# Performance work log

Hardware: AMD Instinct MI355X
Metric: run time of the kernel (lower is better)

## Reference

```python
import jax, jax.numpy as jnp
import numpy as np

H = 512    # hidden size
NF = 512   # num_factor
B, S = 128, 64
D0, D1 = 1536, 2048


def setup_inputs() -> dict:
    key = jax.random.key(0)
    ks = jax.random.split(key, 14)
    stdv = 1.0 / np.sqrt(H)
    u = lambda k, shape: jax.random.uniform(k, shape, jnp.float32, -stdv, stdv)
    return {
        "x0": jax.random.normal(ks[0], (B, S, D0), jnp.float32),  # auxiliary stream (skip_info=1)
        "x1": jax.random.normal(ks[1], (B, S, D1), jnp.float32),  # main encoded stream
        # SVD_Weights for stream 0 (num_gate=2, no individual part) -> weight_fh
        "wa0": u(ks[2], (2 * H, NF)),
        "wb0": jax.random.uniform(ks[3], (NF, 1), jnp.float32, 1 - stdv, 1 + stdv),
        "wc0": u(ks[4], (NF, D0)),
        "b0": u(ks[5], (2 * H,)),
        # SVD_Weights for stream 1 (num_gate=2 shared + individual) -> weight_ih
        "wa1": u(ks[6], (2 * H, NF)),
        "wb1": jax.random.uniform(ks[7], (NF, 1), jnp.float32, 1 - stdv, 1 + stdv),
        "wc1": u(ks[8], (NF, D1)),
        "b1": u(ks[9], (2 * H,)),
        "iw1": u(ks[10], (H, D1)),
        "ib1": u(ks[11], (H,)),
        # GRU hidden-to-hidden params
        "whh": u(ks[12], (3 * H, H)),
        "bhh": u(ks[13], (3 * H,)),
    }


def _svd_weight(wa, wb, wc):
    # tag = [[1.]] (length_tag == 1)  ->  mid = wb @ tag = wb[:, 0]
    # W = wa @ diag(mid) @ wc
    return (wa * wb[:, 0][None, :]) @ wc


def reference(x0, x1, wa0, wb0, wc0, b0, wa1, wb1, wc1, b1, iw1, ib1, whh, bhh):
    bsz = x1.shape[0]
    # get_all_params for stream 1: [2H shared gates; H individual n-gate]
    w_ih = jnp.concatenate([_svd_weight(wa1, wb1, wc1), iw1], axis=0)  # [3H, D1]
    b_ih = jnp.concatenate([b1, ib1], axis=0)                          # [3H]
    # get_shared_params for stream 0: auxiliary gate contributions
    w_fh = _svd_weight(wa0, wb0, wc0)                                  # [2H, D0]

    # Precompute all input-side projections (time-parallel GEMMs)
    gi = jnp.einsum('bsd,gd->bsg', x1, w_ih) + b_ih   # [B,S,3H]
    gf = jnp.einsum('bsd,gd->bsg', x0, w_fh) + b0     # [B,S,2H]
    i_r, i_i, i_n = jnp.split(gi, 3, axis=-1)
    f_r, f_i = jnp.split(gf, 2, axis=-1)

    def step(hx, xs):
        ir, ii, inn, fr, fi = xs
        gh = hx @ whh.T + bhh
        h_r, h_i, h_n = jnp.split(gh, 3, axis=-1)
        r = jax.nn.sigmoid(ir + h_r + fr)
        z = jax.nn.sigmoid(ii + h_i + fi)
        n = jnp.tanh(inn + r * h_n)
        hy = n + z * (hx - n)
        return hy, hy

    xs = tuple(jnp.swapaxes(a, 0, 1) for a in (i_r, i_i, i_n, f_r, f_i))  # time-major
    h0 = jnp.zeros((bsz, H), x1.dtype)
    hT, out = jax.lax.scan(step, h0, xs)
    return jnp.swapaxes(out, 0, 1), hT  # ([B,S,H], [B,H])
```

## Files before the change

### kernel.cpp

```cpp
#include <hip/hip_runtime.h>

#define AS1 __attribute__((address_space(1)))
#define AS3 __attribute__((address_space(3)))

typedef __attribute__((ext_vector_type(8))) short short8;
typedef __attribute__((ext_vector_type(4))) float f32x4;
typedef __attribute__((ext_vector_type(4))) int int4v;
typedef unsigned long long u64;

static __device__ __forceinline__ unsigned short f2bf(float f) {
    unsigned u = __builtin_bit_cast(unsigned, f);
    u += 0x7FFFu + ((u >> 16) & 1u);
    return (unsigned short)(u >> 16);
}


__global__ void cvt_bf16_kernel(const float* __restrict__ in,
                                unsigned short* __restrict__ out, int n8) {
    int i = blockIdx.x * blockDim.x + threadIdx.x;
    int stride = gridDim.x * blockDim.x;
    for (; i < n8; i += stride) {
        const float4* p = (const float4*)in + 2 * (size_t)i;
        float4 a = p[0], b = p[1];
        short8 o;
        o[0] = f2bf(a.x); o[1] = f2bf(a.y); o[2] = f2bf(a.z); o[3] = f2bf(a.w);
        o[4] = f2bf(b.x); o[5] = f2bf(b.y); o[6] = f2bf(b.z); o[7] = f2bf(b.w);
        *(short8*)(out + 8 * (size_t)i) = o;
    }
}

__global__ void wab_kernel(const float* __restrict__ wa, const float* __restrict__ wb,
                           unsigned short* __restrict__ out, int n8) {
    int i = blockIdx.x * blockDim.x + threadIdx.x;
    int stride = gridDim.x * blockDim.x;
    for (; i < n8; i += stride) {
        int base = i * 8;
        int k = base & 511;
        const float4* pa = (const float4*)(wa + base);
        const float4* pb = (const float4*)(wb + k);
        float4 a0 = pa[0], a1 = pa[1], b0 = pb[0], b1 = pb[1];
        short8 o;
        o[0] = f2bf(a0.x * b0.x); o[1] = f2bf(a0.y * b0.y);
        o[2] = f2bf(a0.z * b0.z); o[3] = f2bf(a0.w * b0.w);
        o[4] = f2bf(a1.x * b1.x); o[5] = f2bf(a1.y * b1.y);
        o[6] = f2bf(a1.z * b1.z); o[7] = f2bf(a1.w * b1.w);
        *(short8*)(out + 8 * (size_t)i) = o;
    }
}

__global__ void wcT_kernel(const float* __restrict__ wc,
                           unsigned short* __restrict__ out, int N) {
    int i = blockIdx.x * blockDim.x + threadIdx.x;
    int total = N * 512;
    int stride = gridDim.x * blockDim.x;
    for (; i < total; i += stride) {
        int n = i >> 9, k = i & 511;
        out[i] = f2bf(wc[(size_t)k * N + n]);
    }
}

__global__ void bih_kernel(const float* __restrict__ b1, const float* __restrict__ ib1,
                           float* __restrict__ out) {
    int i = blockIdx.x * blockDim.x + threadIdx.x;
    if (i < 1536) out[i] = (i < 1024) ? b1[i] : ib1[i - 1024];
}

__global__ void scan_init_kernel(unsigned short* __restrict__ hbf,
                                 unsigned* __restrict__ ctrl) {
    int i = blockIdx.x * blockDim.x + threadIdx.x;
    if (i < 65536) hbf[i] = 0;
    if (i < 256) ctrl[i] = 0;
}


template <typename OutT, bool BIAS>
__global__ __launch_bounds__(256) void gemm_nt_kernel(
    const unsigned short* __restrict__ A, const unsigned short* __restrict__ B,
    OutT* __restrict__ C, const float* __restrict__ bias, int K, int ldC) {
    __shared__ __align__(16) unsigned short As[128 * 64];
    __shared__ __align__(16) unsigned short Bs[128 * 64];
    const int tid = threadIdx.x;
    const int wave = tid >> 6, lane = tid & 63;
    const long bm = (long)blockIdx.x * 128, bn = (long)blockIdx.y * 128;
    const int wr = (wave >> 1) * 64, wc = (wave & 1) * 64;
    f32x4 acc[4][4] = {};

    const int srow = tid >> 3;
    const int scol = (tid & 7) * 8;
    const unsigned short* Ag = A + bm * K + scol;
    const unsigned short* Bg = B + bn * K + scol;

    for (int kt = 0; kt < K; kt += 64) {
        __syncthreads();
#pragma unroll
        for (int i = 0; i < 4; ++i) {
            __builtin_amdgcn_global_load_lds(
                (const AS1 void*)(Ag + (long)(i * 32 + srow) * K + kt),
                (AS3 void*)(As + i * 2048 + wave * 512), 16, 0, 0);
        }
#pragma unroll
        for (int i = 0; i < 4; ++i) {
            __builtin_amdgcn_global_load_lds(
                (const AS1 void*)(Bg + (long)(i * 32 + srow) * K + kt),
                (AS3 void*)(Bs + i * 2048 + wave * 512), 16, 0, 0);
        }
        __syncthreads();
#pragma unroll
        for (int kk = 0; kk < 2; ++kk) {
            const int ko = kk * 32 + (lane >> 4) * 8;
            short8 af[4], bfr[4];
#pragma unroll
            for (int mi = 0; mi < 4; ++mi)
                af[mi] = *(const short8*)(As + (wr + mi * 16 + (lane & 15)) * 64 + ko);
#pragma unroll
            for (int ni = 0; ni < 4; ++ni)
                bfr[ni] = *(const short8*)(Bs + (wc + ni * 16 + (lane & 15)) * 64 + ko);
#pragma unroll
            for (int mi = 0; mi < 4; ++mi)
#pragma unroll
                for (int ni = 0; ni < 4; ++ni)
                    acc[mi][ni] = __builtin_amdgcn_mfma_f32_16x16x32_bf16(
                        af[mi], bfr[ni], acc[mi][ni], 0, 0, 0);
        }
    }

    const int rbase = (lane >> 4) * 4;
    const int cbase = lane & 15;
#pragma unroll
    for (int mi = 0; mi < 4; ++mi) {
#pragma unroll
        for (int ni = 0; ni < 4; ++ni) {
            long gc = bn + wc + ni * 16 + cbase;
            float bv = BIAS ? bias[gc] : 0.f;
#pragma unroll
            for (int j = 0; j < 4; ++j) {
                long gr = bm + wr + mi * 16 + rbase + j;
                float v = acc[mi][ni][j] + bv;
                if constexpr (sizeof(OutT) == 2)
                    C[gr * ldC + gc] = (OutT)f2bf(v);
                else
                    C[gr * ldC + gc] = v;
            }
        }
    }
}


__global__ __launch_bounds__(256, 1) void gru_scan_kernel(
    unsigned short* __restrict__ hbuf,
    const unsigned short* __restrict__ whh,
    const float* __restrict__ bhh,
    const float* __restrict__ gi, const float* __restrict__ gf,
    float* __restrict__ out, float* __restrict__ hT,
    unsigned* __restrict__ ctrl) {
    __shared__ __align__(16) unsigned short h_lds[16 * 512];
    __shared__ __align__(16) float gis[48 * 68];
    __shared__ __align__(16) float gfs[32 * 68];
    __shared__ unsigned fast_sh;

    const int tid = threadIdx.x;
    const int lane = tid & 63;
    const int wv = tid >> 6;
    const int bid = blockIdx.x;
    const int team = bid & 7;
    const int member = bid >> 3;
    const int r0 = team * 16;
    const int cb = member * 64;
    const int c0 = cb + wv * 16;
    const int lrow = lane & 15;
    const int q = lane >> 4;

    unsigned* flags = ctrl;
    unsigned* xcds = ctrl + 64;
    unsigned* probes = ctrl + 128;

    short8 wf[3][16];
#pragma unroll
    for (int g = 0; g < 3; ++g)
#pragma unroll
        for (int kk = 0; kk < 16; ++kk)
            wf[g][kk] = *(const short8*)(whh + (size_t)(g * 512 + c0 + lrow) * 512 + kk * 32 + q * 8);

    unsigned my_xcc;
    asm volatile("s_getreg_b32 %0, hwreg(20, 0, 32)" : "=s"(my_xcc));
    if (tid == 0) {
        probes[bid] = 0x5A5A0000u + (unsigned)bid;
        asm volatile("s_waitcnt vmcnt(0)" ::: "memory");
        __hip_atomic_store(&xcds[bid], my_xcc + 1u,
                           __ATOMIC_RELAXED, __HIP_MEMORY_SCOPE_AGENT);
    }
    {
        unsigned ok = 1;
        if (tid < 8) {
            int tb = tid * 8 + team;
            unsigned xv;
            do {
                xv = __hip_atomic_load(&xcds[tb], __ATOMIC_RELAXED,
                                       __HIP_MEMORY_SCOPE_AGENT);
                if (xv == 0) __builtin_amdgcn_s_sleep(1);
            } while (xv == 0);
            unsigned pv = *(volatile const unsigned*)&probes[tb];
            ok = (xv == my_xcc + 1u) && (pv == 0x5A5A0000u + (unsigned)tb);
        }
        ok = __all((int)ok) ? 1u : 0u;
        if (tid == 0) fast_sh = ok;
        __syncthreads();
    }
    const bool fast = fast_sh != 0;

    const int hc = c0 + lrow;
    const float br = bhh[hc], bz = bhh[512 + hc], bn_ = bhh[1024 + hc];
    const int rb = r0 + q * 4;
    const int lc = wv * 16 + lrow;
    float hprev[4] = {0.f, 0.f, 0.f, 0.f};

    const int chunk_sub = tid >> 4;
    const int u4 = (tid & 15) * 4;
    float4 sl[5];
    auto slab_load = [&](int t) {
#pragma unroll
        for (int k = 0; k < 5; ++k) {
            int chunk = k * 16 + chunk_sub;
            const float* p;
            if (chunk < 48) {
                int bbq = chunk / 3, g = chunk - bbq * 3;
                p = gi + ((size_t)(r0 + bbq) * 64 + t) * 1536 + g * 512 + cb + u4;
            } else {
                int c2 = chunk - 48, bbq = c2 >> 1, g2 = c2 & 1;
                p = gf + ((size_t)(r0 + bbq) * 64 + t) * 1024 + g2 * 512 + cb + u4;
            }
            sl[k] = *(const float4*)p;
        }
    };
    slab_load(0);

    const int srow = tid >> 4;
    const int cpos = tid & 15;
    const int sw = (srow & 7) << 4;

    for (int t = 0; t < 64; ++t) {
        const unsigned short* hin = hbuf + (t & 1) * 65536;

        if (fast) {
            if (t > 0) {
                const int m0 = cpos >> 3;
                const unsigned need = (unsigned)t;
                for (;;) {
                    unsigned v0 = *(volatile const unsigned*)&flags[(m0 + 0) * 8 + team];
                    unsigned v1 = *(volatile const unsigned*)&flags[(m0 + 2) * 8 + team];
                    unsigned v2 = *(volatile const unsigned*)&flags[(m0 + 4) * 8 + team];
                    unsigned v3 = *(volatile const unsigned*)&flags[(m0 + 6) * 8 + team];
                    if (v0 >= need && v1 >= need && v2 >= need && v3 >= need) break;
                    __builtin_amdgcn_s_sleep(1);
                }
            }
            {
                const char* src = (const char*)(hin + (size_t)(r0 + srow) * 512) + cpos * 16;
                int4v h0, h1, h2, h3;
                asm volatile(
                    "global_load_dwordx4 %0, %4, off sc0\n\t"
                    "global_load_dwordx4 %1, %4, off offset:256 sc0\n\t"
                    "global_load_dwordx4 %2, %4, off offset:512 sc0\n\t"
                    "global_load_dwordx4 %3, %4, off offset:768 sc0\n\t"
                    "s_waitcnt vmcnt(0)"
                    : "=&v"(h0), "=&v"(h1), "=&v"(h2), "=&v"(h3)
                    : "v"(src) : "memory");
                __builtin_amdgcn_sched_barrier(0);
                char* dst = (char*)h_lds + srow * 1024;
                *(int4v*)(dst + (((cpos + 0) * 16) ^ sw)) = h0;
                *(int4v*)(dst + (((cpos + 16) * 16) ^ sw)) = h1;
                *(int4v*)(dst + (((cpos + 32) * 16) ^ sw)) = h2;
                *(int4v*)(dst + (((cpos + 48) * 16) ^ sw)) = h3;
            }
        } else {
            if (t > 0 && tid < 64) {
                const unsigned tgt = (unsigned)t;
                for (;;) {
                    unsigned v = __hip_atomic_load(&flags[(lane & 7) * 8 + team],
                                                   __ATOMIC_RELAXED, __HIP_MEMORY_SCOPE_AGENT);
                    if (__all((int)(v >= tgt))) break;
                    __builtin_amdgcn_s_sleep(1);
                }
                __builtin_amdgcn_fence(__ATOMIC_ACQUIRE, "agent");
            }
            __syncthreads();
            {
                const u64* hs = (const u64*)(hin + (size_t)(r0 + srow) * 512);
                u64 hq[8];
#pragma unroll
                for (int k = 0; k < 8; ++k)
                    hq[k] = __hip_atomic_load(hs + cpos + k * 16,
                                              __ATOMIC_RELAXED, __HIP_MEMORY_SCOPE_AGENT);
                char* dst = (char*)h_lds + srow * 1024;
#pragma unroll
                for (int k = 0; k < 8; ++k) {
                    int byte = (cpos + k * 16) * 8;
                    *(u64*)(dst + (byte ^ sw)) = hq[k];
                }
            }
        }

#pragma unroll
        for (int k = 0; k < 5; ++k) {
            int chunk = k * 16 + chunk_sub;
            float* d = (chunk < 48) ? &gis[chunk * 68] : &gfs[(chunk - 48) * 68];
            *(float4*)(d + u4) = sl[k];
        }
        __syncthreads();

        if (!fast && t < 63) slab_load(t + 1);

        f32x4 acc0 = {}, acc1 = {}, acc2 = {};
        {
            const char* hl = (const char*)h_lds + lrow * 1024;
            const int sw2 = (lrow & 7) << 4;
#pragma unroll
            for (int kk = 0; kk < 16; ++kk) {
                short8 a = *(const short8*)(hl + ((kk * 64 + q * 16) ^ sw2));
                acc0 = __builtin_amdgcn_mfma_f32_16x16x32_bf16(a, wf[0][kk], acc0, 0, 0, 0);
                acc1 = __builtin_amdgcn_mfma_f32_16x16x32_bf16(a, wf[1][kk], acc1, 0, 0, 0);
                acc2 = __builtin_amdgcn_mfma_f32_16x16x32_bf16(a, wf[2][kk], acc2, 0, 0, 0);
            }
        }

        float hy4[4];
        unsigned short* hout = hbuf + ((t & 1) ^ 1) * 65536;
#pragma unroll
        for (int j = 0; j < 4; ++j) {
            const int bbq = q * 4 + j;
            float ir  = gis[(bbq * 3 + 0) * 68 + lc];
            float ii  = gis[(bbq * 3 + 1) * 68 + lc];
            float inn = gis[(bbq * 3 + 2) * 68 + lc];
            float fr  = gfs[(bbq * 2 + 0) * 68 + lc];
            float fi  = gfs[(bbq * 2 + 1) * 68 + lc];
            float r = 1.f / (1.f + __expf(-(ir + acc0[j] + br + fr)));
            float z = 1.f / (1.f + __expf(-(ii + acc1[j] + bz + fi)));
            float n = tanhf(inn + r * (acc2[j] + bn_));
            float hy = n + z * (hprev[j] - n);
            hprev[j] = hy;
            hy4[j] = hy;
            if (fast) {
                if (t < 63) hout[(size_t)(rb + j) * 512 + hc] = f2bf(hy);
            } else {
                if (t < 63)
                    __hip_atomic_store(hout + (size_t)(rb + j) * 512 + hc,
                                       (unsigned short)f2bf(hy),
                                       __ATOMIC_RELAXED, __HIP_MEMORY_SCOPE_AGENT);
                __builtin_nontemporal_store(hy, &out[((size_t)(rb + j) * 64 + t) * 512 + hc]);
                if (t == 63)
                    __builtin_nontemporal_store(hy, &hT[(size_t)(rb + j) * 512 + hc]);
            }
        }

        if (fast) {
            if (t < 63) {
                __syncthreads();
                if (tid == 0) *(volatile unsigned*)&flags[bid] = (unsigned)(t + 1);
                slab_load(t + 1);
            }
#pragma unroll
            for (int j = 0; j < 4; ++j)
                out[((size_t)(rb + j) * 64 + t) * 512 + hc] = hy4[j];
            if (t == 63) {
#pragma unroll
                for (int j = 0; j < 4; ++j)
                    hT[(size_t)(rb + j) * 512 + hc] = hy4[j];
            }
        } else {
            if (t < 63) {
                __syncthreads();
                if (tid == 0) {
                    __builtin_amdgcn_fence(__ATOMIC_RELEASE, "agent");
                    __hip_atomic_store(&flags[bid], (unsigned)(t + 1),
                                       __ATOMIC_RELAXED, __HIP_MEMORY_SCOPE_AGENT);
                }
            }
        }
    }
}


extern "C" void kernel_launch(void* const* d_in, const int* in_sizes, int n_in,
                              void* d_out, int out_size, void* d_ws, size_t ws_size,
                              hipStream_t stream) {
    (void)in_sizes; (void)n_in; (void)out_size; (void)ws_size;

    const float* x0  = (const float*)d_in[0];
    const float* x1  = (const float*)d_in[1];
    const float* wa0 = (const float*)d_in[2];
    const float* wb0 = (const float*)d_in[3];
    const float* wc0 = (const float*)d_in[4];
    const float* b0  = (const float*)d_in[5];
    const float* wa1 = (const float*)d_in[6];
    const float* wb1 = (const float*)d_in[7];
    const float* wc1 = (const float*)d_in[8];
    const float* b1  = (const float*)d_in[9];
    const float* iw1 = (const float*)d_in[10];
    const float* ib1 = (const float*)d_in[11];
    const float* whh = (const float*)d_in[12];
    const float* bhh = (const float*)d_in[13];

    float* out = (float*)d_out;
    float* hT  = out + (size_t)128 * 64 * 512;

    char* w = (char*)d_ws;
    auto alloc = [&](size_t bytes) {
        char* p = w;
        w += (bytes + 255) & ~(size_t)255;
        return p;
    };
    unsigned short* x1bf = (unsigned short*)alloc((size_t)8192 * 2048 * 2);
    unsigned short* x0bf = (unsigned short*)alloc((size_t)8192 * 1536 * 2);
    unsigned short* wih  = (unsigned short*)alloc((size_t)1536 * 2048 * 2);
    unsigned short* wfh  = (unsigned short*)alloc((size_t)1024 * 1536 * 2);
    unsigned short* wab0 = (unsigned short*)alloc((size_t)1024 * 512 * 2);
    unsigned short* wab1 = (unsigned short*)alloc((size_t)1024 * 512 * 2);
    unsigned short* wc0T = (unsigned short*)alloc((size_t)1536 * 512 * 2);
    unsigned short* wc1T = (unsigned short*)alloc((size_t)2048 * 512 * 2);
    unsigned short* whhb = (unsigned short*)alloc((size_t)1536 * 512 * 2);
    float* bih = (float*)alloc(1536 * 4);
    unsigned short* hbf = (unsigned short*)alloc((size_t)2 * 65536 * 2);
    unsigned* ctrl = (unsigned*)alloc(256 * 4);
    float* gi  = (float*)alloc((size_t)8192 * 1536 * 4);
    float* gf  = (float*)alloc((size_t)8192 * 1024 * 4);

    cvt_bf16_kernel<<<2048, 256, 0, stream>>>(x1, x1bf, (8192 * 2048) / 8);
    cvt_bf16_kernel<<<2048, 256, 0, stream>>>(x0, x0bf, (8192 * 1536) / 8);
    wab_kernel<<<256, 256, 0, stream>>>(wa0, wb0, wab0, (1024 * 512) / 8);
    wab_kernel<<<256, 256, 0, stream>>>(wa1, wb1, wab1, (1024 * 512) / 8);
    wcT_kernel<<<768, 256, 0, stream>>>(wc0, wc0T, 1536);
    wcT_kernel<<<1024, 256, 0, stream>>>(wc1, wc1T, 2048);
    cvt_bf16_kernel<<<384, 256, 0, stream>>>(whh, whhb, (1536 * 512) / 8);
    cvt_bf16_kernel<<<512, 256, 0, stream>>>(iw1, wih + (size_t)1024 * 2048, (512 * 2048) / 8);
    bih_kernel<<<6, 256, 0, stream>>>(b1, ib1, bih);
    scan_init_kernel<<<256, 256, 0, stream>>>(hbf, ctrl);

    gemm_nt_kernel<unsigned short, false><<<dim3(8, 12), 256, 0, stream>>>(
        wab0, wc0T, wfh, nullptr, 512, 1536);
    gemm_nt_kernel<unsigned short, false><<<dim3(8, 16), 256, 0, stream>>>(
        wab1, wc1T, wih, nullptr, 512, 2048);

    gemm_nt_kernel<float, true><<<dim3(64, 12), 256, 0, stream>>>(
        x1bf, wih, gi, bih, 2048, 1536);
    gemm_nt_kernel<float, true><<<dim3(64, 8), 256, 0, stream>>>(
        x0bf, wfh, gf, b0, 1536, 1024);

    gru_scan_kernel<<<64, 256, 0, stream>>>(hbf, whhb, bhh, gi, gf, out, hT, ctrl);
}
```

Before: 576.9 us.

## Use per-wave progress flags in scan to drop block-wide barrier before publishing

The recurrent GRU scan kernel now publishes one progress flag per wave instead of one per block. Each wave signals as soon as its own h slice is stored, so the __syncthreads before the flag write goes away. Consumer threads poll only the four wave flags covering the h segment they load. The barrier after the LDS slab staging becomes a bare lgkmcnt wait plus s_barrier, so the vmcnt wait does not stall it. This trades more flag polling traffic and a larger ctrl area for finer-grained, earlier cross-block signalling on the serial critical path.

```diff
diff --git a/kernel.cpp b/kernel.cpp
--- a/kernel.cpp
+++ b/kernel.cpp
@@ -69,7 +69,7 @@
                                  unsigned* __restrict__ ctrl) {
     int i = blockIdx.x * blockDim.x + threadIdx.x;
     if (i < 65536) hbf[i] = 0;
-    if (i < 256) ctrl[i] = 0;
+    if (i < 512) ctrl[i] = 0;
 }
 
 
@@ -171,8 +171,8 @@
     const int q = lane >> 4;
 
     unsigned* flags = ctrl;
-    unsigned* xcds = ctrl + 64;
-    unsigned* probes = ctrl + 128;
+    unsigned* xcds = ctrl + 256;
+    unsigned* probes = ctrl + 320;
 
     short8 wf[3][16];
 #pragma unroll
@@ -237,19 +237,24 @@
     const int srow = tid >> 4;
     const int cpos = tid & 15;
     const int sw = (srow & 7) << 4;
+    const unsigned* fwp[4];
+#pragma unroll
+    for (int k = 0; k < 4; ++k) {
+        int seg = (cpos >> 1) + k * 8;
+        fwp[k] = &flags[(((seg >> 2) * 8 + team) << 2) + (seg & 3)];
+    }
 
     for (int t = 0; t < 64; ++t) {
         const unsigned short* hin = hbuf + (t & 1) * 65536;
 
         if (fast) {
             if (t > 0) {
-                const int m0 = cpos >> 3;
                 const unsigned need = (unsigned)t;
                 for (;;) {
-                    unsigned v0 = *(volatile const unsigned*)&flags[(m0 + 0) * 8 + team];
-                    unsigned v1 = *(volatile const unsigned*)&flags[(m0 + 2) * 8 + team];
-                    unsigned v2 = *(volatile const unsigned*)&flags[(m0 + 4) * 8 + team];
-                    unsigned v3 = *(volatile const unsigned*)&flags[(m0 + 6) * 8 + team];
+                    unsigned v0 = *(volatile const unsigned*)fwp[0];
+                    unsigned v1 = *(volatile const unsigned*)fwp[1];
+                    unsigned v2 = *(volatile const unsigned*)fwp[2];
+                    unsigned v3 = *(volatile const unsigned*)fwp[3];
                     if (v0 >= need && v1 >= need && v2 >= need && v3 >= need) break;
                     __builtin_amdgcn_s_sleep(1);
                 }
@@ -276,7 +281,7 @@
             if (t > 0 && tid < 64) {
                 const unsigned tgt = (unsigned)t;
                 for (;;) {
-                    unsigned v = __hip_atomic_load(&flags[(lane & 7) * 8 + team],
+                    unsigned v = __hip_atomic_load(&flags[((lane & 7) * 8 + team) << 2],
                                                    __ATOMIC_RELAXED, __HIP_MEMORY_SCOPE_AGENT);
                     if (__all((int)(v >= tgt))) break;
                     __builtin_amdgcn_s_sleep(1);
@@ -306,9 +311,15 @@
             float* d = (chunk < 48) ? &gis[chunk * 68] : &gfs[(chunk - 48) * 68];
             *(float4*)(d + u4) = sl[k];
         }
-        __syncthreads();
-
-        if (!fast && t < 63) slab_load(t + 1);
+
+        if (fast) {
+            asm volatile("s_waitcnt lgkmcnt(0)" ::: "memory");
+            __builtin_amdgcn_s_barrier();
+            __builtin_amdgcn_sched_barrier(0);
+        } else {
+            __syncthreads();
+            if (t < 63) slab_load(t + 1);
+        }
 
         f32x4 acc0 = {}, acc1 = {}, acc2 = {};
         {
@@ -354,8 +365,10 @@
 
         if (fast) {
             if (t < 63) {
-                __syncthreads();
-                if (tid == 0) *(volatile unsigned*)&flags[bid] = (unsigned)(t + 1);
+                asm volatile("s_waitcnt vmcnt(0)" ::: "memory");
+                __builtin_amdgcn_sched_barrier(0);
+                if (lane == 0)
+                    *(volatile unsigned*)&flags[(bid << 2) + wv] = (unsigned)(t + 1);
                 slab_load(t + 1);
             }
 #pragma unroll
@@ -371,7 +384,7 @@
                 __syncthreads();
                 if (tid == 0) {
                     __builtin_amdgcn_fence(__ATOMIC_RELEASE, "agent");
-                    __hip_atomic_store(&flags[bid], (unsigned)(t + 1),
+                    __hip_atomic_store(&flags[bid << 2], (unsigned)(t + 1),
                                        __ATOMIC_RELAXED, __HIP_MEMORY_SCOPE_AGENT);
                 }
             }
@@ -420,7 +433,7 @@
     unsigned short* whhb = (unsigned short*)alloc((size_t)1536 * 512 * 2);
     float* bih = (float*)alloc(1536 * 4);
     unsigned short* hbf = (unsigned short*)alloc((size_t)2 * 65536 * 2);
-    unsigned* ctrl = (unsigned*)alloc(256 * 4);
+    unsigned* ctrl = (unsigned*)alloc(512 * 4);
     float* gi  = (float*)alloc((size_t)8192 * 1536 * 4);
     float* gf  = (float*)alloc((size_t)8192 * 1024 * 4);
 
```

Measured after the change: 599.7 us. +4.0%, slower.
